# Kernel optimization log

Measured on AMD Instinct MI355X. Metric: run time of the kernel, lower is better.

## Reference

```python
import jax, jax.numpy as jnp
import numpy as np

B, S, D = 2, 2048, 1024
H = 16
HD = D // H  # 64

def setup_inputs() -> dict:
    key = jax.random.key(0)
    ks = jax.random.split(key, 6)
    s = 1.0 / np.sqrt(D)
    return {
        "x": jax.random.normal(ks[0], (B, S, D), dtype=jnp.float32),
        "Wq": jax.random.normal(ks[1], (D, D), dtype=jnp.float32) * s,
        "Wk": jax.random.normal(ks[2], (D, D), dtype=jnp.float32) * s,
        "Wv": jax.random.normal(ks[3], (D, D), dtype=jnp.float32) * s,
        "Wo": jax.random.normal(ks[4], (D, D), dtype=jnp.float32) * s,
        "bo": jax.random.normal(ks[5], (D,), dtype=jnp.float32) * 0.01,
    }

def reference(x, Wq, Wk, Wv, Wo, bo):
    b, n, _ = x.shape
    # qkv projections (nn.Linear: x @ W^T, no bias for qkv)
    q = (x @ Wq.T).reshape(b, n, H, HD).transpose(0, 2, 1, 3)  # [B,H,S,hd]
    k = (x @ Wk.T).reshape(b, n, H, HD).transpose(0, 2, 1, 3)
    v = (x @ Wv.T).reshape(b, n, H, HD).transpose(0, 2, 1, 3)
    scores = jnp.einsum('bhqd,bhkd->bhqk', q, k)  # [B,H,S,S]
    causal = jnp.triu(jnp.ones((n, n), dtype=bool), k=1)
    scores = jnp.where(causal, -jnp.inf, scores)
    attn = jax.nn.softmax(scores / np.sqrt(HD), axis=-1)
    ctx = jnp.einsum('bhqk,bhkd->bhqd', attn, v)  # [B,H,S,hd]
    ctx = ctx.transpose(0, 2, 1, 3).reshape(b, n, D)
    return ctx @ Wo.T + bo
```

## Files before the change

### kernel.cpp

```cpp
#include <hip/hip_runtime.h>
#include <hip/hip_bf16.h>

typedef __hip_bfloat16 bf16;
typedef short v8s __attribute__((ext_vector_type(8)));
typedef float v4f __attribute__((ext_vector_type(4)));

#define S_ 2048
#define D_ 1024
#define H_ 16
#define HD_ 64

#define EXP2F(x) __builtin_amdgcn_exp2f(x)
#define NEG_BIG (-1.0e30f)
#define C2 0.1803368801111244f

#define GLDS16(g, l) __builtin_amdgcn_global_load_lds(                        \
    (const __attribute__((address_space(1))) unsigned int*)(g),               \
    (__attribute__((address_space(3))) unsigned int*)(l), 16, 0, 0)

static __device__ __forceinline__ unsigned short bf16_bits(bf16 h) {
    union { bf16 h; unsigned short u; } c; c.h = h; return c.u;
}

static __device__ __forceinline__ v8s pack_bf16x8(const float4 a, const float4 b) {
    union { v8s v; unsigned short u[8]; } r;
    r.u[0] = bf16_bits(__float2bfloat16(a.x));
    r.u[1] = bf16_bits(__float2bfloat16(a.y));
    r.u[2] = bf16_bits(__float2bfloat16(a.z));
    r.u[3] = bf16_bits(__float2bfloat16(a.w));
    r.u[4] = bf16_bits(__float2bfloat16(b.x));
    r.u[5] = bf16_bits(__float2bfloat16(b.y));
    r.u[6] = bf16_bits(__float2bfloat16(b.z));
    r.u[7] = bf16_bits(__float2bfloat16(b.w));
    return r.v;
}

__global__ __launch_bounds__(256)
void cvt_bf16(const float* __restrict__ x,  const float* __restrict__ wq,
              const float* __restrict__ wk, const float* __restrict__ wv,
              const float* __restrict__ wo,
              bf16* __restrict__ xb,  bf16* __restrict__ wqb,
              bf16* __restrict__ wkb, bf16* __restrict__ wvb,
              bf16* __restrict__ wob)
{
    const int seg = blockIdx.y;
    const float* src; bf16* dst; int n;
    switch (seg) {
        case 0: src = x;  dst = xb;  n = 4096 * 1024; break;
        case 1: src = wq; dst = wqb; n = 1024 * 1024; break;
        case 2: src = wk; dst = wkb; n = 1024 * 1024; break;
        case 3: src = wv; dst = wvb; n = 1024 * 1024; break;
        default:src = wo; dst = wob; n = 1024 * 1024; break;
    }
    const int idx = (blockIdx.x * 256 + threadIdx.x) * 8;
    if (idx >= n) return;
    *(v8s*)&dst[idx] = pack_bf16x8(*(const float4*)&src[idx],
                                   *(const float4*)&src[idx + 4]);
}

static __device__ __forceinline__ void stage_half(bf16* ldsbase, const bf16* gbase,
                                                  int w, int l) {
    const int r = l >> 3, c = ((l & 7) ^ r) * 8;
    GLDS16(gbase + (size_t)((2 * w + 0) * 8 + r) * 1024 + c, ldsbase + (2 * w + 0) * 512);
    GLDS16(gbase + (size_t)((2 * w + 1) * 8 + r) * 1024 + c, ldsbase + (2 * w + 1) * 512);
}

#define MF16(a, b, c) __builtin_amdgcn_mfma_f32_16x16x32_bf16(a, b, c, 0, 0, 0)

#define LDA(buf, mf0) { _Pragma("unroll") for (int m_ = 0; m_ < 4; ++m_) {          \
    af[m_][0] = *(const v8s*)&AsS[(buf)*16384 + abase + ((mf0) + m_)*1024 + sw0];   \
    af[m_][1] = *(const v8s*)&AsS[(buf)*16384 + abase + ((mf0) + m_)*1024 + sw1]; } }
#define LDB0(buf) { _Pragma("unroll") for (int n_ = 0; n_ < 2; ++n_) {              \
    b0f[n_][0] = *(const v8s*)&BsS[(buf)*16384 + bbase + n_*1024 + sw0];            \
    b0f[n_][1] = *(const v8s*)&BsS[(buf)*16384 + bbase + n_*1024 + sw1]; } }
#define LDB1(buf) { _Pragma("unroll") for (int n_ = 0; n_ < 2; ++n_) {              \
    b1f[n_][0] = *(const v8s*)&BsS[(buf)*16384 + bbase + (2 + n_)*1024 + sw0];      \
    b1f[n_][1] = *(const v8s*)&BsS[(buf)*16384 + bbase + (2 + n_)*1024 + sw1]; } }
#define MMQ(MH, NH, AF, BF) { _Pragma("unroll") for (int m_ = 0; m_ < 4; ++m_)      \
    _Pragma("unroll") for (int n_ = 0; n_ < 2; ++n_) {                              \
      acc[(MH)*4 + m_][(NH)*2 + n_] =                                               \
        MF16(AF[m_][0], BF[n_][0], acc[(MH)*4 + m_][(NH)*2 + n_]);                  \
      acc[(MH)*4 + m_][(NH)*2 + n_] =                                               \
        MF16(AF[m_][1], BF[n_][1], acc[(MH)*4 + m_][(NH)*2 + n_]); } }
#define BAR() __builtin_amdgcn_s_barrier()
#define VMC2() asm volatile("s_waitcnt vmcnt(2)" ::: "memory")
#define PRIO1() __builtin_amdgcn_s_setprio(1)
#define PRIO0() __builtin_amdgcn_s_setprio(0)

__global__ __launch_bounds__(512, 2)
void gemm_qkv_8p(const bf16* __restrict__ xb, const bf16* __restrict__ wqb,
                 const bf16* __restrict__ wkb, const bf16* __restrict__ wvb,
                 bf16* __restrict__ qd, bf16* __restrict__ kd, bf16* __restrict__ vtd)
{
    __shared__ bf16 AsS[2 * 16384];
    __shared__ bf16 BsS[2 * 16384];
    const int mode = blockIdx.z;
    const bf16* __restrict__ W = (mode == 0) ? wqb : (mode == 1) ? wkb : wvb;
    const int m0 = blockIdx.x * 256;
    const int n0 = blockIdx.y * 256;
    const int t = threadIdx.x;
    const int lane = t & 63, w = t >> 6;
    const int wr = w >> 2, wc = w & 3;
    const int l15 = lane & 15, quad = lane >> 4;
    const int sw0 = (quad ^ (l15 & 7)) * 8;
    const int sw1 = ((quad + 4) ^ (l15 & 7)) * 8;
    const int abase = wr * 8192 + l15 * 64;
    const int bbase = (wc >> 1) * 8192 + (wc & 1) * 4096 + l15 * 64;
    const bf16* Aap = xb + (size_t)m0 * 1024;
    const bf16* Bbp = W + (size_t)n0 * 1024;

    v4f acc[8][4] = {};
    v8s af[4][2], b0f[2][2], b1f[2][2];

    stage_half(AsS,          Aap,          w, lane);
    stage_half(AsS + 8192,   Aap + 131072, w, lane);
    stage_half(BsS,          Bbp,          w, lane);
    stage_half(BsS + 8192,   Bbp + 131072, w, lane);
    stage_half(AsS + 16384,  Aap + 64,     w, lane);
    VMC2();
    BAR();

    for (int i = 0; i < 8; ++i) {
        const int kc = i * 128;
        LDA(0, 0); LDB0(0);
        stage_half(AsS + 16384 + 8192, Aap + 131072 + kc + 64, w, lane);
        BAR(); PRIO1(); MMQ(0, 0, af, b0f); PRIO0(); BAR();
        LDB1(0);
        stage_half(BsS + 16384, Bbp + kc + 64, w, lane);
        BAR(); PRIO1(); MMQ(0, 1, af, b1f); PRIO0(); BAR();
        LDA(0, 4);
        stage_half(BsS + 16384 + 8192, Bbp + 131072 + kc + 64, w, lane);
        BAR(); PRIO1(); MMQ(1, 1, af, b1f); PRIO0(); BAR();
        stage_half(AsS, Aap + kc + 128, w, lane);
        VMC2();
        BAR(); PRIO1(); MMQ(1, 0, af, b0f); PRIO0(); BAR();
        LDA(1, 0); LDB0(1);
        stage_half(AsS + 8192, Aap + 131072 + kc + 128, w, lane);
        BAR(); PRIO1(); MMQ(0, 0, af, b0f); PRIO0(); BAR();
        LDB1(1);
        stage_half(BsS, Bbp + kc + 128, w, lane);
        BAR(); PRIO1(); MMQ(0, 1, af, b1f); PRIO0(); BAR();
        LDA(1, 4);
        stage_half(BsS + 8192, Bbp + 131072 + kc + 128, w, lane);
        BAR(); PRIO1(); MMQ(1, 1, af, b1f); PRIO0(); BAR();
        stage_half(AsS + 16384, Aap + kc + 192, w, lane);
        VMC2();
        BAR(); PRIO1(); MMQ(1, 0, af, b0f); PRIO0(); BAR();
    }

    const float qscale = (mode == 0) ? C2 : 1.0f;
#pragma unroll
    for (int mf = 0; mf < 8; ++mf) {
        const int mb = m0 + wr * 128 + mf * 16 + quad * 4;
        const int b_ = mb >> 11, s = mb & 2047;
#pragma unroll
        for (int nf = 0; nf < 4; ++nf) {
            const int n = n0 + wc * 64 + nf * 16 + l15;
            const int h = n >> 6, d = n & 63;
            if (mode == 2) {
                unsigned int lo = (unsigned int)bf16_bits(__float2bfloat16(acc[mf][nf][0]))
                                | ((unsigned int)bf16_bits(__float2bfloat16(acc[mf][nf][1])) << 16);
                unsigned int hi = (unsigned int)bf16_bits(__float2bfloat16(acc[mf][nf][2]))
                                | ((unsigned int)bf16_bits(__float2bfloat16(acc[mf][nf][3])) << 16);
                uint2 pv; pv.x = lo; pv.y = hi;
                *(uint2*)&vtd[((b_ * H_ + h) * HD_ + d) * S_ + s] = pv;
            } else {
                bf16* __restrict__ dst = (mode == 0) ? qd : kd;
#pragma unroll
                for (int r = 0; r < 4; ++r)
                    dst[((b_ * H_ + h) * S_ + (s + r)) * HD_ + d] =
                        __float2bfloat16(acc[mf][nf][r] * qscale);
            }
        }
    }
}

__global__ __launch_bounds__(256)
void gemm_out_f(const bf16* __restrict__ ctx, const bf16* __restrict__ wob,
                const float* __restrict__ bo, float* __restrict__ out)
{
    const int m0 = blockIdx.x * 128;
    const int n0 = blockIdx.y * 128;
    __shared__ bf16 As[128 * 32];
    __shared__ bf16 Bs[128 * 32];
    const int t    = threadIdx.x;
    const int lane = t & 63, w = t >> 6;
    const int wr = w >> 1, wc = w & 1;
    const int l15 = lane & 15, quad = lane >> 4;
    const int r16 = lane >> 2, c8 = (lane & 3) * 8;
    v4f acc[4][4] = {};

    const bf16* ga = &ctx[(m0 + w*16 + r16) * 1024 + c8];
    const bf16* gb = &wob[(n0 + w*16 + r16) * 1024 + c8];
    bf16* la0 = &As[w * 16 * 32];
    bf16* la1 = &As[(64 + w * 16) * 32];
    bf16* lb0 = &Bs[w * 16 * 32];
    bf16* lb1 = &Bs[(64 + w * 16) * 32];

    for (int k0 = 0; k0 < 1024; k0 += 32) {
        __syncthreads();
        GLDS16(ga + k0,             la0);
        GLDS16(ga + k0 + 64 * 1024, la1);
        GLDS16(gb + k0,             lb0);
        GLDS16(gb + k0 + 64 * 1024, lb1);
        __syncthreads();
        v8s a[4], b[4];
#pragma unroll
        for (int mt = 0; mt < 4; mt++) a[mt] = *(const v8s*)&As[(wr*64 + mt*16 + l15)*32 + quad*8];
#pragma unroll
        for (int nt = 0; nt < 4; nt++) b[nt] = *(const v8s*)&Bs[(wc*64 + nt*16 + l15)*32 + quad*8];
#pragma unroll
        for (int mt = 0; mt < 4; mt++)
#pragma unroll
            for (int nt = 0; nt < 4; nt++)
                acc[mt][nt] = __builtin_amdgcn_mfma_f32_16x16x32_bf16(a[mt], b[nt], acc[mt][nt], 0, 0, 0);
    }

#pragma unroll
    for (int mt = 0; mt < 4; mt++) {
        const int mb = m0 + wr*64 + mt*16 + quad*4;
#pragma unroll
        for (int nt = 0; nt < 4; nt++) {
            const int n = n0 + wc*64 + nt*16 + l15;
            const float bias = bo[n];
#pragma unroll
            for (int r = 0; r < 4; r++)
                out[(mb + r)*1024 + n] = acc[mt][nt][r] + bias;
        }
    }
}

__global__ __launch_bounds__(256)
void gemm_qkv(const float* __restrict__ x, const float* __restrict__ Wq,
              const float* __restrict__ Wk, const float* __restrict__ Wv,
              bf16* __restrict__ qd, bf16* __restrict__ kd, bf16* __restrict__ vtd)
{
    const int mode = blockIdx.z;
    const float* __restrict__ W = (mode == 0) ? Wq : (mode == 1) ? Wk : Wv;
    const int m0 = blockIdx.x * 128;
    const int n0 = blockIdx.y * 128;
    __shared__ bf16 As[128 * 40];
    __shared__ bf16 Bs[128 * 40];
    const int t    = threadIdx.x;
    const int lane = t & 63, w = t >> 6;
    const int wr = w >> 1, wc = w & 1;
    const int l15 = lane & 15, quad = lane >> 4;
    const int srow = t >> 2, scol = (t & 3) * 8;
    v4f acc[4][4] = {};

    for (int k0 = 0; k0 < 1024; k0 += 32) {
        __syncthreads();
        {
            const float* pa = &x[(m0 + srow) * 1024 + k0 + scol];
            *(v8s*)&As[srow*40 + scol] = pack_bf16x8(*(const float4*)pa, *(const float4*)(pa + 4));
            const float* pa2 = pa + 64 * 1024;
            *(v8s*)&As[(srow+64)*40 + scol] = pack_bf16x8(*(const float4*)pa2, *(const float4*)(pa2 + 4));
            const float* pb = &W[(n0 + srow) * 1024 + k0 + scol];
            *(v8s*)&Bs[srow*40 + scol] = pack_bf16x8(*(const float4*)pb, *(const float4*)(pb + 4));
            const float* pb2 = pb + 64 * 1024;
            *(v8s*)&Bs[(srow+64)*40 + scol] = pack_bf16x8(*(const float4*)pb2, *(const float4*)(pb2 + 4));
        }
        __syncthreads();
        v8s a[4], b[4];
#pragma unroll
        for (int mt = 0; mt < 4; mt++) a[mt] = *(const v8s*)&As[(wr*64 + mt*16 + l15)*40 + quad*8];
#pragma unroll
        for (int nt = 0; nt < 4; nt++) b[nt] = *(const v8s*)&Bs[(wc*64 + nt*16 + l15)*40 + quad*8];
#pragma unroll
        for (int mt = 0; mt < 4; mt++)
#pragma unroll
            for (int nt = 0; nt < 4; nt++)
                acc[mt][nt] = __builtin_amdgcn_mfma_f32_16x16x32_bf16(a[mt], b[nt], acc[mt][nt], 0, 0, 0);
    }

    const float qscale = (mode == 0) ? C2 : 1.0f;
#pragma unroll
    for (int mt = 0; mt < 4; mt++) {
        const int mb = m0 + wr*64 + mt*16 + quad*4;
        const int b_ = mb >> 11, s = mb & 2047;
#pragma unroll
        for (int nt = 0; nt < 4; nt++) {
            const int n = n0 + wc*64 + nt*16 + l15;
            const int h = n >> 6, d = n & 63;
            if (mode == 2) {
                unsigned int lo = (unsigned int)bf16_bits(__float2bfloat16(acc[mt][nt][0]))
                                | ((unsigned int)bf16_bits(__float2bfloat16(acc[mt][nt][1])) << 16);
                unsigned int hi = (unsigned int)bf16_bits(__float2bfloat16(acc[mt][nt][2]))
                                | ((unsigned int)bf16_bits(__float2bfloat16(acc[mt][nt][3])) << 16);
                uint2 pv; pv.x = lo; pv.y = hi;
                *(uint2*)&vtd[((b_*H_ + h)*HD_ + d)*S_ + s] = pv;
            } else {
                bf16* __restrict__ dst = (mode == 0) ? qd : kd;
#pragma unroll
                for (int r = 0; r < 4; r++)
                    dst[((b_*H_ + h)*S_ + (s + r))*HD_ + d] = __float2bfloat16(acc[mt][nt][r] * qscale);
            }
        }
    }
}

__global__ __launch_bounds__(256)
void gemm_out(const bf16* __restrict__ ctx, const float* __restrict__ Wo,
              const float* __restrict__ bo, float* __restrict__ out)
{
    const int m0 = blockIdx.x * 128;
    const int n0 = blockIdx.y * 128;
    __shared__ bf16 As[128 * 40];
    __shared__ bf16 Bs[128 * 40];
    const int t    = threadIdx.x;
    const int lane = t & 63, w = t >> 6;
    const int wr = w >> 1, wc = w & 1;
    const int l15 = lane & 15, quad = lane >> 4;
    const int srow = t >> 2, scol = (t & 3) * 8;
    v4f acc[4][4] = {};

    for (int k0 = 0; k0 < 1024; k0 += 32) {
        __syncthreads();
        {
            *(v8s*)&As[srow*40 + scol]      = *(const v8s*)&ctx[(m0+srow)*1024 + k0 + scol];
            *(v8s*)&As[(srow+64)*40 + scol] = *(const v8s*)&ctx[(m0+srow+64)*1024 + k0 + scol];
            const float* pb = &Wo[(n0 + srow) * 1024 + k0 + scol];
            *(v8s*)&Bs[srow*40 + scol] = pack_bf16x8(*(const float4*)pb, *(const float4*)(pb + 4));
            const float* pb2 = pb + 64 * 1024;
            *(v8s*)&Bs[(srow+64)*40 + scol] = pack_bf16x8(*(const float4*)pb2, *(const float4*)(pb2 + 4));
        }
        __syncthreads();
        v8s a[4], b[4];
#pragma unroll
        for (int mt = 0; mt < 4; mt++) a[mt] = *(const v8s*)&As[(wr*64 + mt*16 + l15)*40 + quad*8];
#pragma unroll
        for (int nt = 0; nt < 4; nt++) b[nt] = *(const v8s*)&Bs[(wc*64 + nt*16 + l15)*40 + quad*8];
#pragma unroll
        for (int mt = 0; mt < 4; mt++)
#pragma unroll
            for (int nt = 0; nt < 4; nt++)
                acc[mt][nt] = __builtin_amdgcn_mfma_f32_16x16x32_bf16(a[mt], b[nt], acc[mt][nt], 0, 0, 0);
    }

#pragma unroll
    for (int mt = 0; mt < 4; mt++) {
        const int mb = m0 + wr*64 + mt*16 + quad*4;
#pragma unroll
        for (int nt = 0; nt < 4; nt++) {
            const int n = n0 + wc*64 + nt*16 + l15;
            const float bias = bo[n];
#pragma unroll
            for (int r = 0; r < 4; r++)
                out[(mb + r)*1024 + n] = acc[mt][nt][r] + bias;
        }
    }
}

__global__ __launch_bounds__(512)
void flash_attn(const bf16* __restrict__ qd, const bf16* __restrict__ kd,
                const bf16* __restrict__ vtd, bf16* __restrict__ ctx)
{
    const int bh = blockIdx.x;
    const int p  = blockIdx.y;
    const int t = threadIdx.x;
    const int lane = t & 63, w = t >> 6;
    const int l15 = lane & 15, quad = lane >> 4;
    const int side = w >> 2, wl = w & 3;
    const int q0 = (side ? (15 - p) : p) * 128;
    const int nT = 16 - p;

    __shared__ bf16 Vs[2][64 * 136];
    __shared__ bf16 Pl[8][16 * 72];

    const int mrow0 = q0 + wl * 16;
    const int mrow1 = q0 + 64 + wl * 16;

    v8s qf[2][2];
#pragma unroll
    for (int mt = 0; mt < 2; mt++) {
        const bf16* qb_ = qd + (bh*S_ + (mt ? mrow1 : mrow0) + l15) * HD_;
        qf[mt][0] = *(const v8s*)(qb_ + quad*8);
        qf[mt][1] = *(const v8s*)(qb_ + 32 + quad*8);
    }

    v4f o[2][4] = {};
    float ps[2][4] = {};

    const int vrow = t >> 3, vcol = (t & 7) * 8;
    const bf16* vp = vtd + (bh*HD_ + vrow)*S_ + vcol;
    v8s pv0 = *(const v8s*)vp;
    v8s pv1 = *(const v8s*)(vp + 64);

    const bf16* kbase = kd + (size_t)bh * S_ * HD_;
    v8s kf[4][2];
#pragma unroll
    for (int kt = 0; kt < 4; kt++) {
        const bf16* kp_ = kbase + (kt*16 + l15)*HD_ + quad*8;
        kf[kt][0] = *(const v8s*)kp_;
        kf[kt][1] = *(const v8s*)(kp_ + 32);
    }

    for (int it = 0; it < nT; ++it) {
        const int c0 = it * 128;
        bf16* Vb = &Vs[it & 1][0];
        *(v8s*)&Vb[vrow*136 + vcol]      = pv0;
        *(v8s*)&Vb[vrow*136 + 64 + vcol] = pv1;
        __syncthreads();
        vp += 128;
        pv0 = *(const v8s*)vp;
        pv1 = *(const v8s*)(vp + 64);

#pragma unroll
        for (int h = 0; h < 2; ++h) {
            const int ch = c0 + h * 64;
            const bool act  = (ch      <= mrow1 + 15);
            const bool nact = (ch + 64 <= mrow1 + 15);
            v8s nkf[4][2];
            if (nact) {
#pragma unroll
                for (int kt = 0; kt < 4; kt++) {
                    const bf16* kp_ = kbase + (ch + 64 + kt*16 + l15)*HD_ + quad*8;
                    nkf[kt][0] = *(const v8s*)kp_;
                    nkf[kt][1] = *(const v8s*)(kp_ + 32);
                }
            }

            if (act) {
                v8s vf[4][2];
#pragma unroll
                for (int dt = 0; dt < 4; dt++) {
                    vf[dt][0] = *(const v8s*)&Vb[(dt*16 + l15)*136 + h*64 + quad*8];
                    vf[dt][1] = *(const v8s*)&Vb[(dt*16 + l15)*136 + h*64 + 32 + quad*8];
                }

#pragma unroll
                for (int mt = 0; mt < 2; mt++) {
                    const int mr = mt ? mrow1 : mrow0;
                    if (ch > mr + 15) continue;
                    v4f sc[4] = {};
#pragma unroll
                    for (int kt = 0; kt < 4; kt++) {
                        sc[kt] = __builtin_amdgcn_mfma_f32_16x16x32_bf16(qf[mt][0], kf[kt][0], sc[kt], 0, 0, 0);
                        sc[kt] = __builtin_amdgcn_mfma_f32_16x16x32_bf16(qf[mt][1], kf[kt][1], sc[kt], 0, 0, 0);
                    }
                    const bool full = (ch + 63 <= mr);
#pragma unroll
                    for (int r = 0; r < 4; r++) {
                        const int qg = mr + quad*4 + r;
#pragma unroll
                        for (int kt = 0; kt < 4; kt++) {
                            float s = sc[kt][r];
                            if (!full) {
                                const int kg = ch + kt*16 + l15;
                                s = (kg <= qg) ? s : NEG_BIG;
                            }
                            const float pp = EXP2F(s);
                            sc[kt][r] = pp;
                            ps[mt][r] += pp;
                        }
                    }
                    bf16* pw = &Pl[w][0];
#pragma unroll
                    for (int kt = 0; kt < 4; kt++)
#pragma unroll
                        for (int r = 0; r < 4; r++)
                            pw[(quad*4 + r)*72 + kt*16 + l15] = __float2bfloat16(sc[kt][r]);
                    v8s pf0 = *(const v8s*)&pw[l15*72 + quad*8];
                    v8s pf1 = *(const v8s*)&pw[l15*72 + 32 + quad*8];
#pragma unroll
                    for (int dt = 0; dt < 4; dt++) {
                        o[mt][dt] = __builtin_amdgcn_mfma_f32_16x16x32_bf16(pf0, vf[dt][0], o[mt][dt], 0, 0, 0);
                        o[mt][dt] = __builtin_amdgcn_mfma_f32_16x16x32_bf16(pf1, vf[dt][1], o[mt][dt], 0, 0, 0);
                    }
                }
            }
            if (nact) {
#pragma unroll
                for (int kt = 0; kt < 4; kt++) { kf[kt][0] = nkf[kt][0]; kf[kt][1] = nkf[kt][1]; }
            }
        }
    }

    const int b_ = bh >> 4, hh = bh & 15;
#pragma unroll
    for (int mt = 0; mt < 2; mt++) {
        const int mr = mt ? mrow1 : mrow0;
#pragma unroll
        for (int r = 0; r < 4; r++) {
            float l = ps[mt][r];
#pragma unroll
            for (int off = 1; off < 16; off <<= 1) l += __shfl_xor(l, off);
            const float linv = 1.0f / l;
            const int qg = mr + quad*4 + r;
#pragma unroll
            for (int dt = 0; dt < 4; dt++)
                ctx[(b_*S_ + qg)*D_ + hh*HD_ + dt*16 + l15] = __float2bfloat16(o[mt][dt][r] * linv);
        }
    }
}

extern "C" void kernel_launch(void* const* d_in, const int* in_sizes, int n_in,
                              void* d_out, int out_size, void* d_ws, size_t ws_size,
                              hipStream_t stream) {
    const float* x  = (const float*)d_in[0];
    const float* Wq = (const float*)d_in[1];
    const float* Wk = (const float*)d_in[2];
    const float* Wv = (const float*)d_in[3];
    const float* Wo = (const float*)d_in[4];
    const float* bo = (const float*)d_in[5];
    float* out = (float*)d_out;

    const size_t SEG = (size_t)2 * H_ * S_ * HD_;
    bf16* qd  = (bf16*)d_ws;
    bf16* kd  = qd  + SEG;
    bf16* vtd = kd  + SEG;
    bf16* xc  = vtd + SEG;
    bf16* wqb = xc + SEG;
    bf16* wkb = wqb + 1024 * 1024;
    bf16* wvb = wkb + 1024 * 1024;
    bf16* wob = wvb + 1024 * 1024;

    const size_t need_fast = (4 * SEG + 4 * 1024 * 1024) * sizeof(bf16);

    if (ws_size >= need_fast) {
        cvt_bf16<<<dim3(2048, 5), 256, 0, stream>>>(x, Wq, Wk, Wv, Wo,
                                                    xc, wqb, wkb, wvb, wob);
        gemm_qkv_8p<<<dim3(16, 4, 3), 512, 0, stream>>>(xc, wqb, wkb, wvb, qd, kd, vtd);
        flash_attn<<<dim3(32, 8), 512, 0, stream>>>(qd, kd, vtd, xc);
        gemm_out_f<<<dim3(32, 8), 256, 0, stream>>>(xc, wob, bo, out);
    } else {
        gemm_qkv<<<dim3(32, 8, 3), 256, 0, stream>>>(x, Wq, Wk, Wv, qd, kd, vtd);
        flash_attn<<<dim3(32, 8), 512, 0, stream>>>(qd, kd, vtd, xc);
        gemm_out<<<dim3(32, 8), 256, 0, stream>>>(xc, Wo, bo, out);
    }
}
```

Measured before the change: 199.3 us.

## Rewrite flash attention inner loop with 32x32 MFMA and register-resident P

```diff
diff --git a/kernel.cpp b/kernel.cpp
--- a/kernel.cpp
+++ b/kernel.cpp
@@ -4,6 +4,7 @@
 typedef __hip_bfloat16 bf16;
 typedef short v8s __attribute__((ext_vector_type(8)));
 typedef float v4f __attribute__((ext_vector_type(4)));
+typedef float v16f __attribute__((ext_vector_type(16)));
 
 #define S_ 2048
 #define D_ 1024
@@ -17,6 +18,14 @@
 #define GLDS16(g, l) __builtin_amdgcn_global_load_lds(                        \
     (const __attribute__((address_space(1))) unsigned int*)(g),               \
     (__attribute__((address_space(3))) unsigned int*)(l), 16, 0, 0)
+
+#define CVT_PK(d, lo, hi) \
+    asm("v_cvt_pk_bf16_f32 %0, %1, %2" : "=v"(d) : "v"(lo), "v"(hi))
+
+#define SWAPHALF(a, b) \
+    asm("v_permlane32_swap_b32 %0, %1" : "+v"(a), "+v"(b))
+
+#define MFMA32(a, b, c) __builtin_amdgcn_mfma_f32_32x32x16_bf16(a, b, c, 0, 0, 0)
 
 static __device__ __forceinline__ unsigned short bf16_bits(bf16 h) {
     union { bf16 h; unsigned short u; } c; c.h = h; return c.u;
@@ -351,6 +360,41 @@
     }
 }
 
+#define SOFTMAX_PV(sa, ks0, vA0, vA1, vB0, vB1)                                \
+    {                                                                          \
+        const bool full_ = ((ks0) + 31 <= q0w);                                \
+        if (full_) {                                                           \
+            _Pragma("unroll")                                                  \
+            for (int r = 0; r < 16; r++) {                                     \
+                const float p = EXP2F(sa[r]); sa[r] = p;                       \
+                if (r & 1) ps1 += p; else ps0 += p;                            \
+            }                                                                  \
+        } else {                                                               \
+            const int kb_ = (ks0) + 4 * hi - q0w - l31;                        \
+            _Pragma("unroll")                                                  \
+            for (int r = 0; r < 16; r++) {                                     \
+                const int kl_ = (r & 3) + 8 * (r >> 2);                        \
+                const float p = EXP2F((kb_ + kl_ <= 0) ? sa[r] : NEG_BIG);     \
+                sa[r] = p;                                                     \
+                if (r & 1) ps1 += p; else ps0 += p;                            \
+            }                                                                  \
+        }                                                                      \
+        unsigned u0, u1, u2, u3, u4, u5, u6, u7;                               \
+        CVT_PK(u0, sa[0],  sa[1]);  CVT_PK(u1, sa[2],  sa[3]);                 \
+        CVT_PK(u2, sa[4],  sa[5]);  CVT_PK(u3, sa[6],  sa[7]);                 \
+        CVT_PK(u4, sa[8],  sa[9]);  CVT_PK(u5, sa[10], sa[11]);                \
+        CVT_PK(u6, sa[12], sa[13]); CVT_PK(u7, sa[14], sa[15]);                \
+        SWAPHALF(u0, u2); SWAPHALF(u1, u3);                                    \
+        SWAPHALF(u4, u6); SWAPHALF(u5, u7);                                    \
+        union { v8s v; unsigned w[4]; } pa0_, pa1_;                            \
+        pa0_.w[0] = u0; pa0_.w[1] = u1; pa0_.w[2] = u2; pa0_.w[3] = u3;        \
+        pa1_.w[0] = u4; pa1_.w[1] = u5; pa1_.w[2] = u6; pa1_.w[3] = u7;        \
+        o0 = MFMA32(pa0_.v, vA0, o0);                                          \
+        o1 = MFMA32(pa0_.v, vB0, o1);                                          \
+        o0 = MFMA32(pa1_.v, vA1, o0);                                          \
+        o1 = MFMA32(pa1_.v, vB1, o1);                                          \
+    }
+
 __global__ __launch_bounds__(512)
 void flash_attn(const bf16* __restrict__ qd, const bf16* __restrict__ kd,
                 const bf16* __restrict__ vtd, bf16* __restrict__ ctx)
@@ -359,41 +403,36 @@
     const int p  = blockIdx.y;
     const int t = threadIdx.x;
     const int lane = t & 63, w = t >> 6;
-    const int l15 = lane & 15, quad = lane >> 4;
+    const int l31 = lane & 31, hi = lane >> 5;
     const int side = w >> 2, wl = w & 3;
-    const int q0 = (side ? (15 - p) : p) * 128;
+    const int q0w = (side ? (15 - p) : p) * 128 + wl * 32;
     const int nT = 16 - p;
 
     __shared__ bf16 Vs[2][64 * 136];
-    __shared__ bf16 Pl[8][16 * 72];
-
-    const int mrow0 = q0 + wl * 16;
-    const int mrow1 = q0 + 64 + wl * 16;
-
-    v8s qf[2][2];
-#pragma unroll
-    for (int mt = 0; mt < 2; mt++) {
-        const bf16* qb_ = qd + (bh*S_ + (mt ? mrow1 : mrow0) + l15) * HD_;
-        qf[mt][0] = *(const v8s*)(qb_ + quad*8);
-        qf[mt][1] = *(const v8s*)(qb_ + 32 + quad*8);
-    }
-
-    v4f o[2][4] = {};
-    float ps[2][4] = {};
+
+    const bf16* qp = qd + ((size_t)bh * S_ + q0w + l31) * HD_ + hi * 8;
+    const v8s qf0 = *(const v8s*)(qp);
+    const v8s qf1 = *(const v8s*)(qp + 16);
+    const v8s qf2 = *(const v8s*)(qp + 32);
+    const v8s qf3 = *(const v8s*)(qp + 48);
+
+    v16f o0 = {}, o1 = {};
+    float ps0 = 0.f, ps1 = 0.f;
 
     const int vrow = t >> 3, vcol = (t & 7) * 8;
-    const bf16* vp = vtd + (bh*HD_ + vrow)*S_ + vcol;
+    const bf16* vp = vtd + ((size_t)bh * HD_ + vrow) * S_ + vcol;
     v8s pv0 = *(const v8s*)vp;
     v8s pv1 = *(const v8s*)(vp + 64);
 
-    const bf16* kbase = kd + (size_t)bh * S_ * HD_;
-    v8s kf[4][2];
-#pragma unroll
-    for (int kt = 0; kt < 4; kt++) {
-        const bf16* kp_ = kbase + (kt*16 + l15)*HD_ + quad*8;
-        kf[kt][0] = *(const v8s*)kp_;
-        kf[kt][1] = *(const v8s*)(kp_ + 32);
-    }
+    const bf16* kq = kd + ((size_t)bh * S_ + l31) * HD_ + hi * 8;
+    v8s kA0 = *(const v8s*)(kq);
+    v8s kA1 = *(const v8s*)(kq + 16);
+    v8s kA2 = *(const v8s*)(kq + 32);
+    v8s kA3 = *(const v8s*)(kq + 48);
+    v8s kB0 = *(const v8s*)(kq + 32 * HD_);
+    v8s kB1 = *(const v8s*)(kq + 32 * HD_ + 16);
+    v8s kB2 = *(const v8s*)(kq + 32 * HD_ + 32);
+    v8s kB3 = *(const v8s*)(kq + 32 * HD_ + 48);
 
     for (int it = 0; it < nT; ++it) {
         const int c0 = it * 128;
@@ -408,89 +447,65 @@
 #pragma unroll
         for (int h = 0; h < 2; ++h) {
             const int ch = c0 + h * 64;
-            const bool act  = (ch      <= mrow1 + 15);
-            const bool nact = (ch + 64 <= mrow1 + 15);
-            v8s nkf[4][2];
+            const bool actA = (ch      <= q0w + 31);
+            const bool actB = (ch + 32 <= q0w + 31);
+            const bool nact = (ch + 64 <= q0w + 31);
+
+            v16f sa0 = {}, sa1 = {};
+            if (actA) {
+                sa0 = MFMA32(kA0, qf0, sa0);
+                sa0 = MFMA32(kA1, qf1, sa0);
+                sa0 = MFMA32(kA2, qf2, sa0);
+                sa0 = MFMA32(kA3, qf3, sa0);
+            }
+            if (actB) {
+                sa1 = MFMA32(kB0, qf0, sa1);
+                sa1 = MFMA32(kB1, qf1, sa1);
+                sa1 = MFMA32(kB2, qf2, sa1);
+                sa1 = MFMA32(kB3, qf3, sa1);
+            }
+
             if (nact) {
-#pragma unroll
-                for (int kt = 0; kt < 4; kt++) {
-                    const bf16* kp_ = kbase + (ch + 64 + kt*16 + l15)*HD_ + quad*8;
-                    nkf[kt][0] = *(const v8s*)kp_;
-                    nkf[kt][1] = *(const v8s*)(kp_ + 32);
-                }
-            }
-
-            if (act) {
-                v8s vf[4][2];
-#pragma unroll
-                for (int dt = 0; dt < 4; dt++) {
-                    vf[dt][0] = *(const v8s*)&Vb[(dt*16 + l15)*136 + h*64 + quad*8];
-                    vf[dt][1] = *(const v8s*)&Vb[(dt*16 + l15)*136 + h*64 + 32 + quad*8];
-                }
-
-#pragma unroll
-                for (int mt = 0; mt < 2; mt++) {
-                    const int mr = mt ? mrow1 : mrow0;
-                    if (ch > mr + 15) continue;
-                    v4f sc[4] = {};
-#pragma unroll
-                    for (int kt = 0; kt < 4; kt++) {
-                        sc[kt] = __builtin_amdgcn_mfma_f32_16x16x32_bf16(qf[mt][0], kf[kt][0], sc[kt], 0, 0, 0);
-                        sc[kt] = __builtin_amdgcn_mfma_f32_16x16x32_bf16(qf[mt][1], kf[kt][1], sc[kt], 0, 0, 0);
-                    }
-                    const bool full = (ch + 63 <= mr);
-#pragma unroll
-                    for (int r = 0; r < 4; r++) {
-                        const int qg = mr + quad*4 + r;
-#pragma unroll
-                        for (int kt = 0; kt < 4; kt++) {
-                            float s = sc[kt][r];
-                            if (!full) {
-                                const int kg = ch + kt*16 + l15;
-                                s = (kg <= qg) ? s : NEG_BIG;
-                            }
-                            const float pp = EXP2F(s);
-                            sc[kt][r] = pp;
-                            ps[mt][r] += pp;
-                        }
-                    }
-                    bf16* pw = &Pl[w][0];
-#pragma unroll
-                    for (int kt = 0; kt < 4; kt++)
-#pragma unroll
-                        for (int r = 0; r < 4; r++)
-                            pw[(quad*4 + r)*72 + kt*16 + l15] = __float2bfloat16(sc[kt][r]);
-                    v8s pf0 = *(const v8s*)&pw[l15*72 + quad*8];
-                    v8s pf1 = *(const v8s*)&pw[l15*72 + 32 + quad*8];
-#pragma unroll
-                    for (int dt = 0; dt < 4; dt++) {
-                        o[mt][dt] = __builtin_amdgcn_mfma_f32_16x16x32_bf16(pf0, vf[dt][0], o[mt][dt], 0, 0, 0);
-                        o[mt][dt] = __builtin_amdgcn_mfma_f32_16x16x32_bf16(pf1, vf[dt][1], o[mt][dt], 0, 0, 0);
-                    }
-                }
-            }
-            if (nact) {
-#pragma unroll
-                for (int kt = 0; kt < 4; kt++) { kf[kt][0] = nkf[kt][0]; kf[kt][1] = nkf[kt][1]; }
-            }
-        }
-    }
-
+                const bf16* kn = kq + (size_t)(ch + 64) * HD_;
+                kA0 = *(const v8s*)(kn);
+                kA1 = *(const v8s*)(kn + 16);
+                kA2 = *(const v8s*)(kn + 32);
+                kA3 = *(const v8s*)(kn + 48);
+                kB0 = *(const v8s*)(kn + 32 * HD_);
+                kB1 = *(const v8s*)(kn + 32 * HD_ + 16);
+                kB2 = *(const v8s*)(kn + 32 * HD_ + 32);
+                kB3 = *(const v8s*)(kn + 32 * HD_ + 48);
+            }
+
+            if (actA) {
+                const int kb = h * 64;
+                const v8s vA0 = *(const v8s*)&Vb[ l31      *136 + kb      + hi*8];
+                const v8s vA1 = *(const v8s*)&Vb[ l31      *136 + kb + 16 + hi*8];
+                const v8s vB0 = *(const v8s*)&Vb[(l31 + 32)*136 + kb      + hi*8];
+                const v8s vB1 = *(const v8s*)&Vb[(l31 + 32)*136 + kb + 16 + hi*8];
+                SOFTMAX_PV(sa0, ch, vA0, vA1, vB0, vB1);
+            }
+            if (actB) {
+                const int kb = h * 64 + 32;
+                const v8s vA2 = *(const v8s*)&Vb[ l31      *136 + kb      + hi*8];
+                const v8s vA3 = *(const v8s*)&Vb[ l31      *136 + kb + 16 + hi*8];
+                const v8s vB2 = *(const v8s*)&Vb[(l31 + 32)*136 + kb      + hi*8];
+                const v8s vB3 = *(const v8s*)&Vb[(l31 + 32)*136 + kb + 16 + hi*8];
+                SOFTMAX_PV(sa1, ch + 32, vA2, vA3, vB2, vB3);
+            }
+        }
+    }
+
+    const float ps = ps0 + ps1;
+    const float tot = ps + __shfl_xor(ps, 32);
     const int b_ = bh >> 4, hh = bh & 15;
-#pragma unroll
-    for (int mt = 0; mt < 2; mt++) {
-        const int mr = mt ? mrow1 : mrow0;
-#pragma unroll
-        for (int r = 0; r < 4; r++) {
-            float l = ps[mt][r];
-#pragma unroll
-            for (int off = 1; off < 16; off <<= 1) l += __shfl_xor(l, off);
-            const float linv = 1.0f / l;
-            const int qg = mr + quad*4 + r;
-#pragma unroll
-            for (int dt = 0; dt < 4; dt++)
-                ctx[(b_*S_ + qg)*D_ + hh*HD_ + dt*16 + l15] = __float2bfloat16(o[mt][dt][r] * linv);
-        }
+    bf16* cb = ctx + ((size_t)b_ * S_ + q0w) * D_ + hh * HD_ + l31;
+#pragma unroll
+    for (int r = 0; r < 16; r++) {
+        const int qr = (r & 3) + 8 * (r >> 2) + 4 * hi;
+        const float linv = 1.0f / __shfl(tot, qr);
+        cb[(size_t)qr * D_]      = __float2bfloat16(o0[r] * linv);
+        cb[(size_t)qr * D_ + 32] = __float2bfloat16(o1[r] * linv);
     }
 }
 
```

Result: faster. 187.8 us (median of 3 runs) (-5.8%).
